# Kernel tuning notes

Measured on AMD Instinct MI355X. Metric: run time of the kernel, lower is better.

Reference implementation:

```python
import jax, jax.numpy as jnp
import numpy as np

D_MODEL = 1024
NUM_HEADS = 16
HEAD_DIM = D_MODEL // NUM_HEADS
N = 4096


def setup_inputs() -> dict:
    key = jax.random.key(0)
    k_x, k_wqkv, k_bqkv, k_wo, k_bo = jax.random.split(key, 5)
    s_in = 1.0 / np.sqrt(D_MODEL)
    return {
        "x": jax.random.normal(k_x, (N, D_MODEL), dtype=jnp.float32),
        "w_qkv": jax.random.uniform(k_wqkv, (D_MODEL, 3 * D_MODEL), jnp.float32, -s_in, s_in),
        "b_qkv": jax.random.uniform(k_bqkv, (3 * D_MODEL,), jnp.float32, -s_in, s_in),
        "w_out": jax.random.uniform(k_wo, (D_MODEL, D_MODEL), jnp.float32, -s_in, s_in),
        "b_out": jax.random.uniform(k_bo, (D_MODEL,), jnp.float32, -s_in, s_in),
    }


def reference(x, w_qkv, b_qkv, w_out, b_out) -> jnp.ndarray:
    n, d = x.shape
    scale = HEAD_DIM ** -0.5
    # fused QKV projection: [N, 3D] -> [3, H, N, hd]
    qkv = (x @ w_qkv + b_qkv).reshape(n, 3, NUM_HEADS, HEAD_DIM).transpose(1, 2, 0, 3)
    q, k, v = qkv[0], qkv[1], qkv[2]
    attn = jax.nn.softmax(jnp.einsum("hnd,hmd->hnm", q, k) * scale, axis=-1)
    out = jnp.einsum("hnm,hmd->hnd", attn, v)  # [H, N, hd]
    out = out.transpose(1, 0, 2).reshape(n, d)
    return out @ w_out + b_out
```

## Files before the change

### kernel.cpp

```cpp
#include <hip/hip_runtime.h>
#include <hip/hip_bf16.h>

using bf16_t = __bf16;
using bf16x4 = __attribute__((ext_vector_type(4))) __bf16;
using bf16x8 = __attribute__((ext_vector_type(8))) __bf16;
using f32x4  = __attribute__((ext_vector_type(4))) float;
using f32x16 = __attribute__((ext_vector_type(16))) float;
using u32x2  = __attribute__((ext_vector_type(2))) unsigned;

#define N_TOK 4096
#define DM    1024
#define NH    16
#define HD    64
#define D3    3072

__device__ __forceinline__ void gl_lds16(const void* g, void* l) {
  __builtin_amdgcn_global_load_lds((const __attribute__((address_space(1))) void*)g,
                                   (__attribute__((address_space(3))) void*)l, 16, 0, 0);
}

__device__ __forceinline__ unsigned pkbf(float a, float b) {
  unsigned short la = __builtin_bit_cast(unsigned short, (bf16_t)a);
  unsigned short lb = __builtin_bit_cast(unsigned short, (bf16_t)b);
  return (unsigned)la | ((unsigned)lb << 16);
}

__device__ __forceinline__ bf16x8 mk8(unsigned a, unsigned b, unsigned c, unsigned d) {
  union { unsigned u[4]; bf16x8 v; } t;
  t.u[0] = a; t.u[1] = b; t.u[2] = c; t.u[3] = d;
  return t.v;
}

__device__ __forceinline__ void softmax_blk(const f32x16& sv, bf16x8& apA, bf16x8& apB) {
  float pp[16];
  #pragma unroll
  for (int r = 0; r < 16; r++) pp[r] = exp2f(sv[r]);
  unsigned w00 = pkbf(pp[0], pp[1]),   w01 = pkbf(pp[2], pp[3]);
  unsigned w10 = pkbf(pp[4], pp[5]),   w11 = pkbf(pp[6], pp[7]);
  unsigned w20 = pkbf(pp[8], pp[9]),   w21 = pkbf(pp[10], pp[11]);
  unsigned w30 = pkbf(pp[12], pp[13]), w31 = pkbf(pp[14], pp[15]);
  u32x2 r00 = __builtin_amdgcn_permlane32_swap(w00, w10, false, false);
  u32x2 r01 = __builtin_amdgcn_permlane32_swap(w01, w11, false, false);
  u32x2 r10 = __builtin_amdgcn_permlane32_swap(w20, w30, false, false);
  u32x2 r11 = __builtin_amdgcn_permlane32_swap(w21, w31, false, false);
  apA = mk8(r00[0], r01[0], r00[1], r01[1]);
  apB = mk8(r10[0], r11[0], r10[1], r11[1]);
}

__global__ void k_cvt_x(const float* __restrict__ x, bf16_t* __restrict__ xb) {
  int i = (blockIdx.x * blockDim.x + threadIdx.x) * 8;
  float4 f0 = *(const float4*)(x + i);
  float4 f1 = *(const float4*)(x + i + 4);
  bf16x8 v;
  v[0] = (bf16_t)f0.x; v[1] = (bf16_t)f0.y; v[2] = (bf16_t)f0.z; v[3] = (bf16_t)f0.w;
  v[4] = (bf16_t)f1.x; v[5] = (bf16_t)f1.y; v[6] = (bf16_t)f1.z; v[7] = (bf16_t)f1.w;
  *(bf16x8*)(xb + i) = v;
}

__global__ void k_transpose_cvt(const float* __restrict__ in, bf16_t* __restrict__ outh,
                                int R, int C) {
  __shared__ float tile[64][65];
  int r0 = blockIdx.y * 64, c0 = blockIdx.x * 64;
  int t = threadIdx.x;
  #pragma unroll
  for (int i = 0; i < 16; i++) {
    int idx = i * 256 + t; int r = idx >> 6, c = idx & 63;
    tile[r][c] = in[(size_t)(r0 + r) * C + (c0 + c)];
  }
  __syncthreads();
  #pragma unroll
  for (int i = 0; i < 16; i++) {
    int idx = i * 256 + t; int c = idx >> 6, r = idx & 63;
    outh[(size_t)(c0 + c) * R + (r0 + r)] = (bf16_t)tile[r][c];
  }
}

__global__ __launch_bounds__(256) void k_gemm_qkv(
    const bf16_t* __restrict__ A, const bf16_t* __restrict__ Bt,
    const float* __restrict__ bias, bf16_t* __restrict__ qkv, bf16_t* __restrict__ vT) {
  __shared__ bf16_t As[128 * 32];
  __shared__ bf16_t Bs[128 * 32];
  const int tid = threadIdx.x, wid = tid >> 6, lane = tid & 63;
  const int bid = blockIdx.x;
  const int brow = bid & 31;
  const int bcol = bid >> 5;
  const int wr = wid >> 1, wc = wid & 1;
  const int lrow = lane & 15, lk = (lane >> 4) * 8;

  f32x4 acc[4][4] = {};

  const int c0 = wid * 64 + lane;
  const int c1 = 256 + wid * 64 + lane;
  const bf16_t* Ab = A + (size_t)(brow * 128) * DM;
  const bf16_t* Bb = Bt + (size_t)(bcol * 128) * DM;

  for (int k0 = 0; k0 < DM; k0 += 32) {
    gl_lds16(Ab + (size_t)(c0 >> 2) * DM + k0 + (c0 & 3) * 8, As + (wid * 64) * 8);
    gl_lds16(Ab + (size_t)(c1 >> 2) * DM + k0 + (c1 & 3) * 8, As + (256 + wid * 64) * 8);
    gl_lds16(Bb + (size_t)(c0 >> 2) * DM + k0 + (c0 & 3) * 8, Bs + (wid * 64) * 8);
    gl_lds16(Bb + (size_t)(c1 >> 2) * DM + k0 + (c1 & 3) * 8, Bs + (256 + wid * 64) * 8);
    __syncthreads();
    bf16x8 a[4], b[4];
    #pragma unroll
    for (int m = 0; m < 4; m++) a[m] = *(const bf16x8*)(As + (wr * 64 + m * 16 + lrow) * 32 + lk);
    #pragma unroll
    for (int n = 0; n < 4; n++) b[n] = *(const bf16x8*)(Bs + (wc * 64 + n * 16 + lrow) * 32 + lk);
    #pragma unroll
    for (int m = 0; m < 4; m++)
      #pragma unroll
      for (int n = 0; n < 4; n++)
        acc[m][n] = __builtin_amdgcn_mfma_f32_16x16x32_bf16(a[m], b[n], acc[m][n], 0, 0, 0);
    __syncthreads();
  }

  const int row0 = brow * 128 + wr * 64, col0 = bcol * 128 + wc * 64;
  #pragma unroll
  for (int n = 0; n < 4; n++) {
    int col = col0 + n * 16 + lrow;
    int which = col >> 10, rem = col & 1023;
    int h = rem >> 6, d = rem & 63;
    float bv = bias[col];
    float scl = (which == 0) ? 0.18033688011112042f : 1.0f;
    if (which == 2) {
      bf16_t* ob = vT + ((size_t)h * HD + d) * N_TOK;
      #pragma unroll
      for (int m = 0; m < 4; m++) {
        int tok0 = row0 + m * 16 + (lane >> 4) * 4;
        bf16x4 pk;
        #pragma unroll
        for (int i = 0; i < 4; i++) pk[i] = (bf16_t)(acc[m][n][i] + bv);
        *(bf16x4*)(ob + tok0) = pk;
      }
    } else {
      bf16_t* ob = qkv + (size_t)(which * NH + h) * N_TOK * HD + d;
      #pragma unroll
      for (int m = 0; m < 4; m++)
        #pragma unroll
        for (int i = 0; i < 4; i++) {
          int row = row0 + m * 16 + (lane >> 4) * 4 + i;
          ob[(size_t)row * HD] = (bf16_t)((acc[m][n][i] + bv) * scl);
        }
    }
  }
}

__global__ __launch_bounds__(256, 4) void k_attn(
    const bf16_t* __restrict__ qkv, const bf16_t* __restrict__ vT,
    float* __restrict__ opart, float* __restrict__ lpart, int kv_chunk) {
  __shared__ bf16_t Kss[2][64 * 64];
  __shared__ bf16_t Vts[2][64 * 64];
  const int tid = threadIdx.x, wid = tid >> 6, lane = tid & 63;
  const int qb = blockIdx.x, h = blockIdx.y, kvs = blockIdx.z;
  const bf16_t* Q  = qkv + (size_t)h * N_TOK * HD;
  const bf16_t* K  = qkv + (size_t)(NH + h) * N_TOK * HD;
  const bf16_t* Vt = vT + (size_t)h * HD * N_TOK;
  const int L31 = lane & 31, h5 = lane >> 5, r7 = L31 & 7;

  const int kv_lo = kvs * kv_chunk;
  const int kv_hi = kv_lo + kv_chunk;

  const int sr0 = tid >> 3;
  const int sc0 = (tid & 7) ^ (sr0 & 7);

#define STAGE(B, KV0) do {                                                                  \
    gl_lds16(K  + (size_t)((KV0) + sr0)      * HD + sc0 * 8, &Kss[B][wid * 512]);           \
    gl_lds16(K  + (size_t)((KV0) + 32 + sr0) * HD + sc0 * 8, &Kss[B][2048 + wid * 512]);    \
    gl_lds16(Vt + (size_t)sr0        * N_TOK + (KV0) + sc0 * 8, &Vts[B][wid * 512]);        \
    gl_lds16(Vt + (size_t)(32 + sr0) * N_TOK + (KV0) + sc0 * 8, &Vts[B][2048 + wid * 512]); \
  } while (0)

  bf16x8 aq[4];
  {
    int qrow = qb * 128 + wid * 32 + L31;
    #pragma unroll
    for (int dc = 0; dc < 4; dc++)
      aq[dc] = *(const bf16x8*)(Q + (size_t)qrow * HD + dc * 16 + h5 * 8);
  }
  f32x16 o0 = {}, o1 = {}, l_acc = {};
  bf16x8 ones8;
  #pragma unroll
  for (int j = 0; j < 8; j++) ones8[j] = (bf16_t)1.0f;

  STAGE(0, kv_lo);
  __syncthreads();

  int buf = 0;
  for (int kv0 = kv_lo; kv0 < kv_hi; kv0 += 64) {
    if (kv0 + 64 < kv_hi) STAGE(buf ^ 1, kv0 + 64);
    const bf16_t* kb = &Kss[buf][0] + L31 * 64;
    const bf16_t* vb = &Vts[buf][0] + L31 * 64;

    f32x16 s0 = {}, s1 = {};
    __builtin_amdgcn_s_setprio(1);
    #pragma unroll
    for (int dc = 0; dc < 4; dc++) {
      bf16x8 kf0 = *(const bf16x8*)(kb + (((dc * 2 + h5) ^ r7) * 8));
      s0 = __builtin_amdgcn_mfma_f32_32x32x16_bf16(kf0, aq[dc], s0, 0, 0, 0);
      bf16x8 kf1 = *(const bf16x8*)(kb + 2048 + (((dc * 2 + h5) ^ r7) * 8));
      s1 = __builtin_amdgcn_mfma_f32_32x32x16_bf16(kf1, aq[dc], s1, 0, 0, 0);
    }
    __builtin_amdgcn_s_setprio(0);

    bf16x8 ap0, ap1, ap2, ap3;
    softmax_blk(s0, ap0, ap1);
    __builtin_amdgcn_s_setprio(1);
    {
      bf16x8 vf;
      vf = *(const bf16x8*)(vb + (((0 + h5) ^ r7) * 8));
      o0 = __builtin_amdgcn_mfma_f32_32x32x16_bf16(ap0, vf, o0, 0, 0, 0);
      vf = *(const bf16x8*)(vb + (((2 + h5) ^ r7) * 8));
      o0 = __builtin_amdgcn_mfma_f32_32x32x16_bf16(ap1, vf, o0, 0, 0, 0);
      vf = *(const bf16x8*)(vb + 2048 + (((0 + h5) ^ r7) * 8));
      o1 = __builtin_amdgcn_mfma_f32_32x32x16_bf16(ap0, vf, o1, 0, 0, 0);
      vf = *(const bf16x8*)(vb + 2048 + (((2 + h5) ^ r7) * 8));
      o1 = __builtin_amdgcn_mfma_f32_32x32x16_bf16(ap1, vf, o1, 0, 0, 0);
      l_acc = __builtin_amdgcn_mfma_f32_32x32x16_bf16(ap0, ones8, l_acc, 0, 0, 0);
      l_acc = __builtin_amdgcn_mfma_f32_32x32x16_bf16(ap1, ones8, l_acc, 0, 0, 0);
    }
    __builtin_amdgcn_s_setprio(0);
    softmax_blk(s1, ap2, ap3);
    __builtin_amdgcn_s_setprio(1);
    {
      bf16x8 vf;
      vf = *(const bf16x8*)(vb + (((4 + h5) ^ r7) * 8));
      o0 = __builtin_amdgcn_mfma_f32_32x32x16_bf16(ap2, vf, o0, 0, 0, 0);
      vf = *(const bf16x8*)(vb + (((6 + h5) ^ r7) * 8));
      o0 = __builtin_amdgcn_mfma_f32_32x32x16_bf16(ap3, vf, o0, 0, 0, 0);
      vf = *(const bf16x8*)(vb + 2048 + (((4 + h5) ^ r7) * 8));
      o1 = __builtin_amdgcn_mfma_f32_32x32x16_bf16(ap2, vf, o1, 0, 0, 0);
      vf = *(const bf16x8*)(vb + 2048 + (((6 + h5) ^ r7) * 8));
      o1 = __builtin_amdgcn_mfma_f32_32x32x16_bf16(ap3, vf, o1, 0, 0, 0);
      l_acc = __builtin_amdgcn_mfma_f32_32x32x16_bf16(ap2, ones8, l_acc, 0, 0, 0);
      l_acc = __builtin_amdgcn_mfma_f32_32x32x16_bf16(ap3, ones8, l_acc, 0, 0, 0);
    }
    __builtin_amdgcn_s_setprio(0);

    __syncthreads();
    buf ^= 1;
  }
#undef STAGE

  if (L31 == 0) {
    float* lp = lpart + ((size_t)kvs * NH + h) * N_TOK + qb * 128 + wid * 32;
    #pragma unroll
    for (int r = 0; r < 16; r++)
      lp[(r & 3) + 8 * (r >> 2) + 4 * h5] = l_acc[r];
  }

  float* op = opart + (size_t)kvs * N_TOK * DM;
  #pragma unroll
  for (int r = 0; r < 16; r++) {
    int q32 = (r & 3) + 8 * (r >> 2) + 4 * h5;
    size_t base = (size_t)(qb * 128 + wid * 32 + q32) * DM + h * HD + L31;
    op[base] = o0[r];
    op[base + 32] = o1[r];
  }
}

__global__ __launch_bounds__(256) void k_combine(
    const float* __restrict__ opart, const float* __restrict__ lpart,
    bf16_t* __restrict__ oattn, int nsplit) {
  const int row = blockIdx.x, tid = threadIdx.x;
  const int col = tid * 4;
  const int h = col >> 6;
  const size_t idx = (size_t)row * DM + col;
  float4 a = *(const float4*)(opart + idx);
  float lsum = lpart[(size_t)h * N_TOK + row];
  if (nsplit == 2) {
    float4 b = *(const float4*)(opart + (size_t)N_TOK * DM + idx);
    a.x += b.x; a.y += b.y; a.z += b.z; a.w += b.w;
    lsum += lpart[(size_t)(NH + h) * N_TOK + row];
  }
  float rl = 1.0f / lsum;
  bf16x4 hv;
  hv[0] = (bf16_t)(a.x * rl); hv[1] = (bf16_t)(a.y * rl);
  hv[2] = (bf16_t)(a.z * rl); hv[3] = (bf16_t)(a.w * rl);
  *(bf16x4*)(oattn + idx) = hv;
}

__global__ __launch_bounds__(256) void k_gemm_out(
    const bf16_t* __restrict__ A, const bf16_t* __restrict__ Bt,
    const float* __restrict__ bias, float* __restrict__ out) {
  __shared__ bf16_t As[128 * 32];
  __shared__ bf16_t Bs[128 * 32];
  const int tid = threadIdx.x, wid = tid >> 6, lane = tid & 63;
  const int bid = blockIdx.x;
  const int brow = bid & 31;
  const int bcol = bid >> 5;
  const int wr = wid >> 1, wc = wid & 1;
  const int lrow = lane & 15, lk = (lane >> 4) * 8;

  f32x4 acc[4][4] = {};

  const int c0 = wid * 64 + lane;
  const int c1 = 256 + wid * 64 + lane;
  const bf16_t* Ab = A + (size_t)(brow * 128) * DM;
  const bf16_t* Bb = Bt + (size_t)(bcol * 128) * DM;

  for (int k0 = 0; k0 < DM; k0 += 32) {
    gl_lds16(Ab + (size_t)(c0 >> 2) * DM + k0 + (c0 & 3) * 8, As + (wid * 64) * 8);
    gl_lds16(Ab + (size_t)(c1 >> 2) * DM + k0 + (c1 & 3) * 8, As + (256 + wid * 64) * 8);
    gl_lds16(Bb + (size_t)(c0 >> 2) * DM + k0 + (c0 & 3) * 8, Bs + (wid * 64) * 8);
    gl_lds16(Bb + (size_t)(c1 >> 2) * DM + k0 + (c1 & 3) * 8, Bs + (256 + wid * 64) * 8);
    __syncthreads();
    bf16x8 a[4], b[4];
    #pragma unroll
    for (int m = 0; m < 4; m++) a[m] = *(const bf16x8*)(As + (wr * 64 + m * 16 + lrow) * 32 + lk);
    #pragma unroll
    for (int n = 0; n < 4; n++) b[n] = *(const bf16x8*)(Bs + (wc * 64 + n * 16 + lrow) * 32 + lk);
    #pragma unroll
    for (int m = 0; m < 4; m++)
      #pragma unroll
      for (int n = 0; n < 4; n++)
        acc[m][n] = __builtin_amdgcn_mfma_f32_16x16x32_bf16(a[m], b[n], acc[m][n], 0, 0, 0);
    __syncthreads();
  }

  const int row0 = brow * 128 + wr * 64, col0 = bcol * 128 + wc * 64;
  #pragma unroll
  for (int n = 0; n < 4; n++) {
    int col = col0 + n * 16 + lrow;
    float bv = bias[col];
    #pragma unroll
    for (int m = 0; m < 4; m++)
      #pragma unroll
      for (int i = 0; i < 4; i++) {
        int row = row0 + m * 16 + (lane >> 4) * 4 + i;
        out[(size_t)row * DM + col] = acc[m][n][i] + bv;
      }
  }
}

extern "C" void kernel_launch(void* const* d_in, const int* in_sizes, int n_in,
                              void* d_out, int out_size, void* d_ws, size_t ws_size,
                              hipStream_t stream) {
  const float* x     = (const float*)d_in[0];
  const float* w_qkv = (const float*)d_in[1];
  const float* b_qkv = (const float*)d_in[2];
  const float* w_out = (const float*)d_in[3];
  const float* b_out = (const float*)d_in[4];
  float* out = (float*)d_out;

  char* ws = (char*)d_ws;
  bf16_t* qkv     = (bf16_t*)(ws);
  bf16_t* x_bf    = (bf16_t*)(ws + 25165824);
  bf16_t* wqkv_t  = (bf16_t*)(ws + 33554432);
  bf16_t* wout_t  = (bf16_t*)(ws + 39845888);
  bf16_t* attn    = (bf16_t*)(ws + 41943040);
  float*  lpart   = (float*)(ws + 50331648);
  float*  opart   = (float*)(ws + 50855936);
  bf16_t* vT      = qkv + (size_t)2 * NH * N_TOK * HD;

  const size_t NEED2 = 84410368ull;
  const int nsplit = (ws_size >= NEED2) ? 2 : 1;

  k_cvt_x<<<2048, 256, 0, stream>>>(x, x_bf);
  k_transpose_cvt<<<dim3(48, 16), 256, 0, stream>>>(w_qkv, wqkv_t, DM, D3);
  k_transpose_cvt<<<dim3(16, 16), 256, 0, stream>>>(w_out, wout_t, DM, DM);
  k_gemm_qkv<<<768, 256, 0, stream>>>(x_bf, wqkv_t, b_qkv, qkv, vT);
  k_attn<<<dim3(32, 16, nsplit), 256, 0, stream>>>(qkv, vT, opart, lpart, N_TOK / nsplit);
  k_combine<<<4096, 256, 0, stream>>>(opart, lpart, attn, nsplit);
  k_gemm_out<<<256, 256, 0, stream>>>(attn, wout_t, b_out, out);
}
```

Baseline: 190.9 us.

## Process two query sub-tiles per wave and sum softmax row totals in VALU

```diff
diff --git a/kernel.cpp b/kernel.cpp
--- a/kernel.cpp
+++ b/kernel.cpp
@@ -31,10 +31,16 @@
   return t.v;
 }
 
-__device__ __forceinline__ void softmax_blk(const f32x16& sv, bf16x8& apA, bf16x8& apB) {
+__device__ __forceinline__ void softmax_blk(const f32x16& sv, float& l_loc,
+                                            bf16x8& apA, bf16x8& apB) {
   float pp[16];
   #pragma unroll
   for (int r = 0; r < 16; r++) pp[r] = exp2f(sv[r]);
+  float t0 = (pp[0] + pp[1]) + (pp[2] + pp[3]);
+  float t1 = (pp[4] + pp[5]) + (pp[6] + pp[7]);
+  float t2 = (pp[8] + pp[9]) + (pp[10] + pp[11]);
+  float t3 = (pp[12] + pp[13]) + (pp[14] + pp[15]);
+  l_loc += (t0 + t1) + (t2 + t3);
   unsigned w00 = pkbf(pp[0], pp[1]),   w01 = pkbf(pp[2], pp[3]);
   unsigned w10 = pkbf(pp[4], pp[5]),   w11 = pkbf(pp[6], pp[7]);
   unsigned w20 = pkbf(pp[8], pp[9]),   w21 = pkbf(pp[10], pp[11]);
@@ -144,11 +150,10 @@
   }
 }
 
-__global__ __launch_bounds__(256, 4) void k_attn(
+__global__ __launch_bounds__(256, 2) void k_attn(
     const bf16_t* __restrict__ qkv, const bf16_t* __restrict__ vT,
     float* __restrict__ opart, float* __restrict__ lpart, int kv_chunk) {
-  __shared__ bf16_t Kss[2][64 * 64];
-  __shared__ bf16_t Vts[2][64 * 64];
+  __shared__ bf16_t smem[4][64 * 64];
   const int tid = threadIdx.x, wid = tid >> 6, lane = tid & 63;
   const int qb = blockIdx.x, h = blockIdx.y, kvs = blockIdx.z;
   const bf16_t* Q  = qkv + (size_t)h * N_TOK * HD;
@@ -157,104 +162,123 @@
   const int L31 = lane & 31, h5 = lane >> 5, r7 = L31 & 7;
 
   const int kv_lo = kvs * kv_chunk;
-  const int kv_hi = kv_lo + kv_chunk;
 
   const int sr0 = tid >> 3;
   const int sc0 = (tid & 7) ^ (sr0 & 7);
 
-#define STAGE(B, KV0) do {                                                                  \
-    gl_lds16(K  + (size_t)((KV0) + sr0)      * HD + sc0 * 8, &Kss[B][wid * 512]);           \
-    gl_lds16(K  + (size_t)((KV0) + 32 + sr0) * HD + sc0 * 8, &Kss[B][2048 + wid * 512]);    \
-    gl_lds16(Vt + (size_t)sr0        * N_TOK + (KV0) + sc0 * 8, &Vts[B][wid * 512]);        \
-    gl_lds16(Vt + (size_t)(32 + sr0) * N_TOK + (KV0) + sc0 * 8, &Vts[B][2048 + wid * 512]); \
+  const bf16_t* gK0 = K + (size_t)(kv_lo + sr0) * HD + sc0 * 8;
+  const bf16_t* gK1 = gK0 + 32 * HD;
+  const bf16_t* gV0 = Vt + (size_t)sr0 * N_TOK + kv_lo + sc0 * 8;
+  const bf16_t* gV1 = gV0 + 32 * N_TOK;
+
+#define STAGE(B) do {                                   \
+    gl_lds16(gK0, &smem[B][wid * 512]);                 \
+    gl_lds16(gK1, &smem[B][2048 + wid * 512]);          \
+    gl_lds16(gV0, &smem[2 + (B)][wid * 512]);           \
+    gl_lds16(gV1, &smem[2 + (B)][2048 + wid * 512]);    \
+    gK0 += 64 * HD; gK1 += 64 * HD; gV0 += 64; gV1 += 64; \
   } while (0)
 
-  bf16x8 aq[4];
-  {
-    int qrow = qb * 128 + wid * 32 + L31;
+  bf16x8 aq[2][4];
+  #pragma unroll
+  for (int qs = 0; qs < 2; qs++) {
+    int qrow = qb * 256 + wid * 64 + qs * 32 + L31;
     #pragma unroll
     for (int dc = 0; dc < 4; dc++)
-      aq[dc] = *(const bf16x8*)(Q + (size_t)qrow * HD + dc * 16 + h5 * 8);
-  }
-  f32x16 o0 = {}, o1 = {}, l_acc = {};
-  bf16x8 ones8;
-  #pragma unroll
-  for (int j = 0; j < 8; j++) ones8[j] = (bf16_t)1.0f;
-
-  STAGE(0, kv_lo);
+      aq[qs][dc] = *(const bf16x8*)(Q + (size_t)qrow * HD + dc * 16 + h5 * 8);
+  }
+
+  const char* kb[4];
+  #pragma unroll
+  for (int dc = 0; dc < 4; dc++)
+    kb[dc] = (const char*)(&smem[0][0] + L31 * 64 + (((dc * 2 + h5) ^ r7) * 8));
+#define LDSRD(base, OFF) (*(const bf16x8*)((base) + (OFF)))
+#define MM(a, b, c) __builtin_amdgcn_mfma_f32_32x32x16_bf16((a), (b), (c), 0, 0, 0)
+
+  f32x16 o[2][2] = {};
+  const f32x16 fz = {};
+  float l_loc[2] = {0.f, 0.f};
+
+  STAGE(0);
   __syncthreads();
 
-  int buf = 0;
-  for (int kv0 = kv_lo; kv0 < kv_hi; kv0 += 64) {
-    if (kv0 + 64 < kv_hi) STAGE(buf ^ 1, kv0 + 64);
-    const bf16_t* kb = &Kss[buf][0] + L31 * 64;
-    const bf16_t* vb = &Vts[buf][0] + L31 * 64;
-
-    f32x16 s0 = {}, s1 = {};
-    __builtin_amdgcn_s_setprio(1);
-    #pragma unroll
-    for (int dc = 0; dc < 4; dc++) {
-      bf16x8 kf0 = *(const bf16x8*)(kb + (((dc * 2 + h5) ^ r7) * 8));
-      s0 = __builtin_amdgcn_mfma_f32_32x32x16_bf16(kf0, aq[dc], s0, 0, 0, 0);
-      bf16x8 kf1 = *(const bf16x8*)(kb + 2048 + (((dc * 2 + h5) ^ r7) * 8));
-      s1 = __builtin_amdgcn_mfma_f32_32x32x16_bf16(kf1, aq[dc], s1, 0, 0, 0);
+#define BODY(B, PRE) do {                                                        \
+    if (PRE) STAGE((B) ^ 1);                                                     \
+    bf16x8 kf0[4], kf1[4];                                                       \
+    _Pragma("unroll")                                                            \
+    for (int dc = 0; dc < 4; dc++) {                                             \
+      kf0[dc] = LDSRD(kb[dc], (B) * 8192);                                       \
+      kf1[dc] = LDSRD(kb[dc], (B) * 8192 + 4096);                                \
+    }                                                                            \
+    bf16x8 pA[4], pB[4];                                                         \
+    {                                                                            \
+      __builtin_amdgcn_s_setprio(1);                                             \
+      f32x16 s0 = MM(kf0[0], aq[0][0], fz);                                      \
+      f32x16 s1 = MM(kf1[0], aq[0][0], fz);                                      \
+      _Pragma("unroll")                                                          \
+      for (int dc = 1; dc < 4; dc++) {                                           \
+        s0 = MM(kf0[dc], aq[0][dc], s0);                                         \
+        s1 = MM(kf1[dc], aq[0][dc], s1);                                         \
+      }                                                                          \
+      __builtin_amdgcn_s_setprio(0);                                             \
+      softmax_blk(s0, l_loc[0], pA[0], pA[1]);                                   \
+      softmax_blk(s1, l_loc[0], pA[2], pA[3]);                                   \
+    }                                                                            \
+    {                                                                            \
+      __builtin_amdgcn_s_setprio(1);                                             \
+      f32x16 s0 = MM(kf0[0], aq[1][0], fz);                                      \
+      f32x16 s1 = MM(kf1[0], aq[1][0], fz);                                      \
+      _Pragma("unroll")                                                          \
+      for (int dc = 1; dc < 4; dc++) {                                           \
+        s0 = MM(kf0[dc], aq[1][dc], s0);                                         \
+        s1 = MM(kf1[dc], aq[1][dc], s1);                                         \
+      }                                                                          \
+      __builtin_amdgcn_s_setprio(0);                                             \
+      softmax_blk(s0, l_loc[1], pB[0], pB[1]);                                   \
+      softmax_blk(s1, l_loc[1], pB[2], pB[3]);                                   \
+    }                                                                            \
+    __builtin_amdgcn_s_setprio(1);                                               \
+    _Pragma("unroll")                                                            \
+    for (int c = 0; c < 4; c++) {                                                \
+      bf16x8 vf0 = LDSRD(kb[c], 16384 + (B) * 8192);                             \
+      bf16x8 vf1 = LDSRD(kb[c], 20480 + (B) * 8192);                             \
+      o[0][0] = MM(pA[c], vf0, o[0][0]);                                         \
+      o[0][1] = MM(pA[c], vf1, o[0][1]);                                         \
+      o[1][0] = MM(pB[c], vf0, o[1][0]);                                         \
+      o[1][1] = MM(pB[c], vf1, o[1][1]);                                         \
+    }                                                                            \
+    __builtin_amdgcn_s_setprio(0);                                               \
+  } while (0)
+
+  const int iters = kv_chunk / 64;
+  for (int it = 0; it < iters; it += 2) {
+    BODY(0, true);
+    __syncthreads();
+    BODY(1, it + 2 < iters);
+    __syncthreads();
+  }
+#undef BODY
+#undef STAGE
+#undef LDSRD
+#undef MM
+
+  #pragma unroll
+  for (int qs = 0; qs < 2; qs++) {
+    float lf = l_loc[qs] + __shfl_xor(l_loc[qs], 32, 64);
+    if (lane < 32)
+      lpart[((size_t)kvs * NH + h) * N_TOK + qb * 256 + wid * 64 + qs * 32 + lane] = lf;
+  }
+
+  float* op = opart + (size_t)kvs * N_TOK * DM;
+  #pragma unroll
+  for (int qs = 0; qs < 2; qs++)
+    #pragma unroll
+    for (int r = 0; r < 16; r++) {
+      int q32 = (r & 3) + 8 * (r >> 2) + 4 * h5;
+      size_t base = (size_t)(qb * 256 + wid * 64 + qs * 32 + q32) * DM + h * HD + L31;
+      op[base] = o[qs][0][r];
+      op[base + 32] = o[qs][1][r];
     }
-    __builtin_amdgcn_s_setprio(0);
-
-    bf16x8 ap0, ap1, ap2, ap3;
-    softmax_blk(s0, ap0, ap1);
-    __builtin_amdgcn_s_setprio(1);
-    {
-      bf16x8 vf;
-      vf = *(const bf16x8*)(vb + (((0 + h5) ^ r7) * 8));
-      o0 = __builtin_amdgcn_mfma_f32_32x32x16_bf16(ap0, vf, o0, 0, 0, 0);
-      vf = *(const bf16x8*)(vb + (((2 + h5) ^ r7) * 8));
-      o0 = __builtin_amdgcn_mfma_f32_32x32x16_bf16(ap1, vf, o0, 0, 0, 0);
-      vf = *(const bf16x8*)(vb + 2048 + (((0 + h5) ^ r7) * 8));
-      o1 = __builtin_amdgcn_mfma_f32_32x32x16_bf16(ap0, vf, o1, 0, 0, 0);
-      vf = *(const bf16x8*)(vb + 2048 + (((2 + h5) ^ r7) * 8));
-      o1 = __builtin_amdgcn_mfma_f32_32x32x16_bf16(ap1, vf, o1, 0, 0, 0);
-      l_acc = __builtin_amdgcn_mfma_f32_32x32x16_bf16(ap0, ones8, l_acc, 0, 0, 0);
-      l_acc = __builtin_amdgcn_mfma_f32_32x32x16_bf16(ap1, ones8, l_acc, 0, 0, 0);
-    }
-    __builtin_amdgcn_s_setprio(0);
-    softmax_blk(s1, ap2, ap3);
-    __builtin_amdgcn_s_setprio(1);
-    {
-      bf16x8 vf;
-      vf = *(const bf16x8*)(vb + (((4 + h5) ^ r7) * 8));
-      o0 = __builtin_amdgcn_mfma_f32_32x32x16_bf16(ap2, vf, o0, 0, 0, 0);
-      vf = *(const bf16x8*)(vb + (((6 + h5) ^ r7) * 8));
-      o0 = __builtin_amdgcn_mfma_f32_32x32x16_bf16(ap3, vf, o0, 0, 0, 0);
-      vf = *(const bf16x8*)(vb + 2048 + (((4 + h5) ^ r7) * 8));
-      o1 = __builtin_amdgcn_mfma_f32_32x32x16_bf16(ap2, vf, o1, 0, 0, 0);
-      vf = *(const bf16x8*)(vb + 2048 + (((6 + h5) ^ r7) * 8));
-      o1 = __builtin_amdgcn_mfma_f32_32x32x16_bf16(ap3, vf, o1, 0, 0, 0);
-      l_acc = __builtin_amdgcn_mfma_f32_32x32x16_bf16(ap2, ones8, l_acc, 0, 0, 0);
-      l_acc = __builtin_amdgcn_mfma_f32_32x32x16_bf16(ap3, ones8, l_acc, 0, 0, 0);
-    }
-    __builtin_amdgcn_s_setprio(0);
-
-    __syncthreads();
-    buf ^= 1;
-  }
-#undef STAGE
-
-  if (L31 == 0) {
-    float* lp = lpart + ((size_t)kvs * NH + h) * N_TOK + qb * 128 + wid * 32;
-    #pragma unroll
-    for (int r = 0; r < 16; r++)
-      lp[(r & 3) + 8 * (r >> 2) + 4 * h5] = l_acc[r];
-  }
-
-  float* op = opart + (size_t)kvs * N_TOK * DM;
-  #pragma unroll
-  for (int r = 0; r < 16; r++) {
-    int q32 = (r & 3) + 8 * (r >> 2) + 4 * h5;
-    size_t base = (size_t)(qb * 128 + wid * 32 + q32) * DM + h * HD + L31;
-    op[base] = o0[r];
-    op[base + 32] = o1[r];
-  }
 }
 
 __global__ __launch_bounds__(256) void k_combine(
@@ -358,7 +382,7 @@
   k_transpose_cvt<<<dim3(48, 16), 256, 0, stream>>>(w_qkv, wqkv_t, DM, D3);
   k_transpose_cvt<<<dim3(16, 16), 256, 0, stream>>>(w_out, wout_t, DM, DM);
   k_gemm_qkv<<<768, 256, 0, stream>>>(x_bf, wqkv_t, b_qkv, qkv, vT);
-  k_attn<<<dim3(32, 16, nsplit), 256, 0, stream>>>(qkv, vT, opart, lpart, N_TOK / nsplit);
+  k_attn<<<dim3(16, 16, nsplit), 256, 0, stream>>>(qkv, vT, opart, lpart, N_TOK / nsplit);
   k_combine<<<4096, 256, 0, stream>>>(opart, lpart, attn, nsplit);
   k_gemm_out<<<256, 256, 0, stream>>>(attn, wout_t, b_out, out);
 }
```

After: 205.5 us. 7.6% more time.

## Load K/V fragments directly from global memory and compute row sums in VALU

Applied to the files above, without the earlier changes.

```diff
diff --git a/kernel.cpp b/kernel.cpp
--- a/kernel.cpp
+++ b/kernel.cpp
@@ -31,10 +31,16 @@
   return t.v;
 }
 
-__device__ __forceinline__ void softmax_blk(const f32x16& sv, bf16x8& apA, bf16x8& apB) {
+__device__ __forceinline__ void softmax_blk(const f32x16& sv, float& l_loc,
+                                            bf16x8& apA, bf16x8& apB) {
   float pp[16];
   #pragma unroll
   for (int r = 0; r < 16; r++) pp[r] = exp2f(sv[r]);
+  float t0 = (pp[0] + pp[1]) + (pp[2] + pp[3]);
+  float t1 = (pp[4] + pp[5]) + (pp[6] + pp[7]);
+  float t2 = (pp[8] + pp[9]) + (pp[10] + pp[11]);
+  float t3 = (pp[12] + pp[13]) + (pp[14] + pp[15]);
+  l_loc += (t0 + t1) + (t2 + t3);
   unsigned w00 = pkbf(pp[0], pp[1]),   w01 = pkbf(pp[2], pp[3]);
   unsigned w10 = pkbf(pp[4], pp[5]),   w11 = pkbf(pp[6], pp[7]);
   unsigned w20 = pkbf(pp[8], pp[9]),   w21 = pkbf(pp[10], pp[11]);
@@ -144,30 +150,17 @@
   }
 }
 
-__global__ __launch_bounds__(256, 4) void k_attn(
+__global__ __launch_bounds__(256, 3) void k_attn(
     const bf16_t* __restrict__ qkv, const bf16_t* __restrict__ vT,
     float* __restrict__ opart, float* __restrict__ lpart, int kv_chunk) {
-  __shared__ bf16_t Kss[2][64 * 64];
-  __shared__ bf16_t Vts[2][64 * 64];
   const int tid = threadIdx.x, wid = tid >> 6, lane = tid & 63;
   const int qb = blockIdx.x, h = blockIdx.y, kvs = blockIdx.z;
+  const int L31 = lane & 31, h5 = lane >> 5;
+  const int kv_lo = kvs * kv_chunk;
+
   const bf16_t* Q  = qkv + (size_t)h * N_TOK * HD;
   const bf16_t* K  = qkv + (size_t)(NH + h) * N_TOK * HD;
   const bf16_t* Vt = vT + (size_t)h * HD * N_TOK;
-  const int L31 = lane & 31, h5 = lane >> 5, r7 = L31 & 7;
-
-  const int kv_lo = kvs * kv_chunk;
-  const int kv_hi = kv_lo + kv_chunk;
-
-  const int sr0 = tid >> 3;
-  const int sc0 = (tid & 7) ^ (sr0 & 7);
-
-#define STAGE(B, KV0) do {                                                                  \
-    gl_lds16(K  + (size_t)((KV0) + sr0)      * HD + sc0 * 8, &Kss[B][wid * 512]);           \
-    gl_lds16(K  + (size_t)((KV0) + 32 + sr0) * HD + sc0 * 8, &Kss[B][2048 + wid * 512]);    \
-    gl_lds16(Vt + (size_t)sr0        * N_TOK + (KV0) + sc0 * 8, &Vts[B][wid * 512]);        \
-    gl_lds16(Vt + (size_t)(32 + sr0) * N_TOK + (KV0) + sc0 * 8, &Vts[B][2048 + wid * 512]); \
-  } while (0)
 
   bf16x8 aq[4];
   {
@@ -176,76 +169,62 @@
     for (int dc = 0; dc < 4; dc++)
       aq[dc] = *(const bf16x8*)(Q + (size_t)qrow * HD + dc * 16 + h5 * 8);
   }
-  f32x16 o0 = {}, o1 = {}, l_acc = {};
-  bf16x8 ones8;
-  #pragma unroll
-  for (int j = 0; j < 8; j++) ones8[j] = (bf16_t)1.0f;
-
-  STAGE(0, kv_lo);
-  __syncthreads();
-
-  int buf = 0;
-  for (int kv0 = kv_lo; kv0 < kv_hi; kv0 += 64) {
-    if (kv0 + 64 < kv_hi) STAGE(buf ^ 1, kv0 + 64);
-    const bf16_t* kb = &Kss[buf][0] + L31 * 64;
-    const bf16_t* vb = &Vts[buf][0] + L31 * 64;
-
-    f32x16 s0 = {}, s1 = {};
+
+  const bf16_t* pK0 = K + (size_t)(kv_lo + L31) * HD + h5 * 8;
+  const bf16_t* pK1 = pK0 + 32 * HD;
+  const bf16_t* pV0 = Vt + (size_t)L31 * N_TOK + kv_lo + h5 * 8;
+  const bf16_t* pV1 = pV0 + (size_t)32 * N_TOK;
+
+#define MM(a, b, c) __builtin_amdgcn_mfma_f32_32x32x16_bf16((a), (b), (c), 0, 0, 0)
+
+  f32x16 o0 = {}, o1 = {};
+  const f32x16 fz = {};
+  float l_loc = 0.f;
+
+  const int iters = kv_chunk / 64;
+  for (int it = 0; it < iters; it++) {
+    bf16x8 kf0[4], kf1[4];
+    #pragma unroll
+    for (int dc = 0; dc < 4; dc++) {
+      kf0[dc] = *(const bf16x8*)(pK0 + dc * 16);
+      kf1[dc] = *(const bf16x8*)(pK1 + dc * 16);
+    }
+    bf16x8 vf0[4], vf1[4];
+    #pragma unroll
+    for (int c = 0; c < 4; c++) {
+      vf0[c] = *(const bf16x8*)(pV0 + c * 16);
+      vf1[c] = *(const bf16x8*)(pV1 + c * 16);
+    }
+
     __builtin_amdgcn_s_setprio(1);
-    #pragma unroll
-    for (int dc = 0; dc < 4; dc++) {
-      bf16x8 kf0 = *(const bf16x8*)(kb + (((dc * 2 + h5) ^ r7) * 8));
-      s0 = __builtin_amdgcn_mfma_f32_32x32x16_bf16(kf0, aq[dc], s0, 0, 0, 0);
-      bf16x8 kf1 = *(const bf16x8*)(kb + 2048 + (((dc * 2 + h5) ^ r7) * 8));
-      s1 = __builtin_amdgcn_mfma_f32_32x32x16_bf16(kf1, aq[dc], s1, 0, 0, 0);
+    f32x16 s0 = MM(kf0[0], aq[0], fz);
+    f32x16 s1 = MM(kf1[0], aq[0], fz);
+    #pragma unroll
+    for (int dc = 1; dc < 4; dc++) {
+      s0 = MM(kf0[dc], aq[dc], s0);
+      s1 = MM(kf1[dc], aq[dc], s1);
     }
     __builtin_amdgcn_s_setprio(0);
 
-    bf16x8 ap0, ap1, ap2, ap3;
-    softmax_blk(s0, ap0, ap1);
+    bf16x8 pA[4];
+    softmax_blk(s0, l_loc, pA[0], pA[1]);
+    softmax_blk(s1, l_loc, pA[2], pA[3]);
+
     __builtin_amdgcn_s_setprio(1);
-    {
-      bf16x8 vf;
-      vf = *(const bf16x8*)(vb + (((0 + h5) ^ r7) * 8));
-      o0 = __builtin_amdgcn_mfma_f32_32x32x16_bf16(ap0, vf, o0, 0, 0, 0);
-      vf = *(const bf16x8*)(vb + (((2 + h5) ^ r7) * 8));
-      o0 = __builtin_amdgcn_mfma_f32_32x32x16_bf16(ap1, vf, o0, 0, 0, 0);
-      vf = *(const bf16x8*)(vb + 2048 + (((0 + h5) ^ r7) * 8));
-      o1 = __builtin_amdgcn_mfma_f32_32x32x16_bf16(ap0, vf, o1, 0, 0, 0);
-      vf = *(const bf16x8*)(vb + 2048 + (((2 + h5) ^ r7) * 8));
-      o1 = __builtin_amdgcn_mfma_f32_32x32x16_bf16(ap1, vf, o1, 0, 0, 0);
-      l_acc = __builtin_amdgcn_mfma_f32_32x32x16_bf16(ap0, ones8, l_acc, 0, 0, 0);
-      l_acc = __builtin_amdgcn_mfma_f32_32x32x16_bf16(ap1, ones8, l_acc, 0, 0, 0);
+    #pragma unroll
+    for (int c = 0; c < 4; c++) {
+      o0 = MM(pA[c], vf0[c], o0);
+      o1 = MM(pA[c], vf1[c], o1);
     }
     __builtin_amdgcn_s_setprio(0);
-    softmax_blk(s1, ap2, ap3);
-    __builtin_amdgcn_s_setprio(1);
-    {
-      bf16x8 vf;
-      vf = *(const bf16x8*)(vb + (((4 + h5) ^ r7) * 8));
-      o0 = __builtin_amdgcn_mfma_f32_32x32x16_bf16(ap2, vf, o0, 0, 0, 0);
-      vf = *(const bf16x8*)(vb + (((6 + h5) ^ r7) * 8));
-      o0 = __builtin_amdgcn_mfma_f32_32x32x16_bf16(ap3, vf, o0, 0, 0, 0);
-      vf = *(const bf16x8*)(vb + 2048 + (((4 + h5) ^ r7) * 8));
-      o1 = __builtin_amdgcn_mfma_f32_32x32x16_bf16(ap2, vf, o1, 0, 0, 0);
-      vf = *(const bf16x8*)(vb + 2048 + (((6 + h5) ^ r7) * 8));
-      o1 = __builtin_amdgcn_mfma_f32_32x32x16_bf16(ap3, vf, o1, 0, 0, 0);
-      l_acc = __builtin_amdgcn_mfma_f32_32x32x16_bf16(ap2, ones8, l_acc, 0, 0, 0);
-      l_acc = __builtin_amdgcn_mfma_f32_32x32x16_bf16(ap3, ones8, l_acc, 0, 0, 0);
-    }
-    __builtin_amdgcn_s_setprio(0);
-
-    __syncthreads();
-    buf ^= 1;
-  }
-#undef STAGE
-
-  if (L31 == 0) {
-    float* lp = lpart + ((size_t)kvs * NH + h) * N_TOK + qb * 128 + wid * 32;
-    #pragma unroll
-    for (int r = 0; r < 16; r++)
-      lp[(r & 3) + 8 * (r >> 2) + 4 * h5] = l_acc[r];
-  }
+
+    pK0 += 64 * HD; pK1 += 64 * HD; pV0 += 64; pV1 += 64;
+  }
+#undef MM
+
+  float lf = l_loc + __shfl_xor(l_loc, 32, 64);
+  if (lane < 32)
+    lpart[((size_t)kvs * NH + h) * N_TOK + qb * 128 + wid * 32 + lane] = lf;
 
   float* op = opart + (size_t)kvs * N_TOK * DM;
   #pragma unroll
```

After: 307.2 us. +60.9%, slower.
